# Optimization experiments

Hardware: AMD Instinct MI355X
Metric: run time of the kernel (lower is better)

## Reference

```python
import jax, jax.numpy as jnp
import numpy as np

M, DIM_X, DIM_Y, PROJ = 4096, 1024, 128, 128
BN_EPS = 1e-5


def setup_inputs() -> dict:
    key = jax.random.key(0)
    ks = jax.random.split(key, 4)
    x = jax.random.normal(ks[0], (M, DIM_X), dtype=jnp.float32)
    y = jax.random.normal(ks[1], (M, DIM_Y), dtype=jnp.float32)
    # BatchNorm1d affine params (init: gamma=1, beta=0)
    bnx_gamma = jnp.ones((DIM_X,), jnp.float32)
    bnx_beta = jnp.zeros((DIM_X,), jnp.float32)
    bny_gamma = jnp.ones((DIM_Y,), jnp.float32)
    bny_beta = jnp.zeros((DIM_Y,), jnp.float32)
    # Linear(dim_x, proj) params
    bound = 1.0 / np.sqrt(DIM_X)
    W = jax.random.uniform(ks[2], (PROJ, DIM_X), jnp.float32, -bound, bound)
    b = jax.random.uniform(ks[3], (PROJ,), jnp.float32, -bound, bound)
    return {"x": x, "y": y, "bnx_gamma": bnx_gamma, "bnx_beta": bnx_beta,
            "bny_gamma": bny_gamma, "bny_beta": bny_beta, "W": W, "b": b}


def _batchnorm(z, gamma, beta):
    # training-mode BatchNorm1d: biased variance over batch dim
    mu = z.mean(axis=0)
    var = z.var(axis=0)
    return (z - mu) * jax.lax.rsqrt(var + BN_EPS) * gamma + beta


def _pairwise_sq_dists(z):
    # -2 z z^T + |z_i|^2 + |z_j|^2  (same formula as the torch module)
    n2 = jnp.sum(z * z, axis=-1, keepdims=True)  # [m,1]
    return -2.0 * (z @ z.T) + n2 + n2.T          # [m,m]


def reference(x, y, bnx_gamma, bnx_beta, bny_gamma, bny_beta, W, b):
    m = x.shape[0]
    xn = _batchnorm(x, bnx_gamma, bnx_beta)
    yn = _batchnorm(y, bny_gamma, bny_beta)
    xp = xn @ W.T + b                              # projected x: [m, PROJ]

    pdx = _pairwise_sq_dists(xp)
    pdy = _pairwise_sq_dists(yn)
    # sigma = max(1e-6, median(pairwise distances).detach())
    sx = jnp.maximum(1e-6, jax.lax.stop_gradient(jnp.median(pdx)))
    sy = jnp.maximum(1e-6, jax.lax.stop_gradient(jnp.median(pdy)))

    K = jnp.exp(-pdx / sx)
    L = jnp.exp(-pdy / sy)
    # trace(L H K H) == sum(L * (H K H)) since L symmetric; H K H = double centering of K
    Kc = K - K.mean(axis=0, keepdims=True) - K.mean(axis=1, keepdims=True) + K.mean()
    hsic = jnp.sum(L * Kc) / ((m - 1) ** 2)
    return hsic
```

## Files before the change

### kernel.cpp

```cpp
#include <hip/hip_runtime.h>


constexpr int   MM  = 4096;
constexpr int   DX  = 1024;
constexpr int   DY  = 128;
constexpr int   PJ  = 128;
constexpr unsigned RANK0 = 8388607u;
constexpr unsigned RANK1 = 8388608u;
constexpr int   NTRI128 = 528;
constexpr int   NTRI64  = 2080;

typedef __attribute__((ext_vector_type(8))) short bf16x8;
typedef __attribute__((ext_vector_type(4))) float f32x4;

struct Ctrl {
  unsigned pref[2];
  unsigned rrank[2];
  float sigma;
  float coef;
};

__device__ __forceinline__ unsigned mapf(float f) {
  unsigned b = __float_as_uint(f);
  return (b & 0x80000000u) ? ~b : (b | 0x80000000u);
}
__device__ __forceinline__ float unmapf(unsigned u) {
  unsigned b = (u & 0x80000000u) ? (u & 0x7fffffffu) : ~u;
  return __uint_as_float(b);
}
__device__ __forceinline__ unsigned short f2bf(float f) {
  unsigned u = __float_as_uint(f);
  return (unsigned short)((u + 0x7fffu + ((u >> 16) & 1u)) >> 16);
}
__device__ __forceinline__ float bf2f(unsigned short h) {
  return __uint_as_float(((unsigned)h) << 16);
}
__device__ __forceinline__ void gload_lds16(const void* g, void* l) {
  __builtin_amdgcn_global_load_lds(
      (const __attribute__((address_space(1))) unsigned int*)g,
      (__attribute__((address_space(3))) unsigned int*)l, 16, 0, 0);
}
__device__ __forceinline__ void tri_map(int lin, int& bi, int& bj) {
  int b = (int)((sqrtf(8.0f * (float)lin + 1.0f) - 1.0f) * 0.5f);
  while ((b + 1) * (b + 2) / 2 <= lin) ++b;
  while (b * (b + 1) / 2 > lin) --b;
  bi = b;
  bj = lin - b * (b + 1) / 2;
}

__global__ void colstats(const float* __restrict__ x, const float* __restrict__ y,
                         double* __restrict__ sumx, double* __restrict__ sqx,
                         double* __restrict__ sumy, double* __restrict__ sqy) {
  const int r0 = blockIdx.y * 256;
  const float* src;
  double *sum, *sq;
  int col, ncols;
  if (blockIdx.x < 4) {
    col = blockIdx.x * 256 + threadIdx.x; ncols = DX; src = x; sum = sumx; sq = sqx;
  } else {
    col = threadIdx.x; ncols = DY; src = y; sum = sumy; sq = sqy;
    if (col >= DY) return;
  }
  const float* px = src + (size_t)r0 * ncols + col;
  double s = 0.0, s2 = 0.0;
  for (int r = 0; r < 256; ++r) {
    float v = *px;
    s  += (double)v;
    s2 += (double)v * (double)v;
    px += ncols;
  }
  atomicAdd(&sum[col], s);
  atomicAdd(&sq[col],  s2);
}

__global__ void finalize_stats(const double* __restrict__ sumx, const double* __restrict__ sqx,
                               const double* __restrict__ sumy, const double* __restrict__ sqy,
                               const float* __restrict__ gx, const float* __restrict__ bx,
                               const float* __restrict__ gy, const float* __restrict__ by,
                               float* __restrict__ axv, float* __restrict__ cxv,
                               float* __restrict__ ayv, float* __restrict__ cyv) {
  const double* sum; const double* sq; const float* gamma; const float* beta;
  float *a, *c; int j;
  if (blockIdx.x < 4) {
    j = blockIdx.x * 256 + threadIdx.x;
    sum = sumx; sq = sqx; gamma = gx; beta = bx; a = axv; c = cxv;
  } else {
    j = threadIdx.x;
    if (j >= DY) return;
    sum = sumy; sq = sqy; gamma = gy; beta = by; a = ayv; c = cyv;
  }
  double mu  = sum[j] * (1.0 / 4096.0);
  double var = sq[j] * (1.0 / 4096.0) - mu * mu;
  float rstd = (float)(1.0 / sqrt(var + 1e-5));
  float aj   = rstd * gamma[j];
  a[j] = aj;
  c[j] = beta[j] - (float)mu * aj;
}

__global__ __launch_bounds__(256) void prep(
    const float* __restrict__ x, const float* __restrict__ y,
    const float* __restrict__ W, const float* __restrict__ b,
    const float* __restrict__ ax, const float* __restrict__ cx,
    const float* __restrict__ ay, const float* __restrict__ cy,
    unsigned short* __restrict__ Ah, unsigned short* __restrict__ Al,
    unsigned short* __restrict__ Wh, unsigned short* __restrict__ Wl,
    unsigned short* __restrict__ Zhy, unsigned short* __restrict__ Zly,
    float* __restrict__ n2y, float* __restrict__ bp) {
  __shared__ float red[256];
  const int bx = blockIdx.x, tid = threadIdx.x;
  if (bx < 4096) {
    int i4 = bx * 256 + tid;
    float4 v = ((const float4*)x)[i4];
    int c0 = (i4 * 4) & 1023;
    v.x *= ax[c0]; v.y *= ax[c0 + 1]; v.z *= ax[c0 + 2]; v.w *= ax[c0 + 3];
    ushort4 h, lo;
    h.x = f2bf(v.x); h.y = f2bf(v.y); h.z = f2bf(v.z); h.w = f2bf(v.w);
    lo.x = f2bf(v.x - bf2f(h.x)); lo.y = f2bf(v.y - bf2f(h.y));
    lo.z = f2bf(v.z - bf2f(h.z)); lo.w = f2bf(v.w - bf2f(h.w));
    ((ushort4*)Ah)[i4] = h;
    ((ushort4*)Al)[i4] = lo;
  } else if (bx < 5120) {
    int wv = tid >> 6, lane = tid & 63;
    int row = (bx - 4096) * 4 + wv;
    size_t base = (size_t)row * 128;
    float v0 = y[base + lane]      * ay[lane]      + cy[lane];
    float v1 = y[base + 64 + lane] * ay[64 + lane] + cy[64 + lane];
    unsigned short h0 = f2bf(v0), h1 = f2bf(v1);
    Zhy[base + lane] = h0;            Zhy[base + 64 + lane] = h1;
    Zly[base + lane] = f2bf(v0 - bf2f(h0));
    Zly[base + 64 + lane] = f2bf(v1 - bf2f(h1));
    float s = v0 * v0 + v1 * v1;
    for (int off = 32; off > 0; off >>= 1) s += __shfl_down(s, off, 64);
    if (lane == 0) n2y[row] = s;
  } else if (bx < 5248) {
    int i4 = (bx - 5120) * 256 + tid;
    float4 v = ((const float4*)W)[i4];
    ushort4 h, lo;
    h.x = f2bf(v.x); h.y = f2bf(v.y); h.z = f2bf(v.z); h.w = f2bf(v.w);
    lo.x = f2bf(v.x - bf2f(h.x)); lo.y = f2bf(v.y - bf2f(h.y));
    lo.z = f2bf(v.z - bf2f(h.z)); lo.w = f2bf(v.w - bf2f(h.w));
    ((ushort4*)Wh)[i4] = h;
    ((ushort4*)Wl)[i4] = lo;
  } else {
    int p = bx - 5248;
    float s = 0.f;
    for (int j = tid; j < DX; j += 256) s += cx[j] * W[(size_t)p * DX + j];
    red[tid] = s; __syncthreads();
    for (int off = 128; off > 0; off >>= 1) {
      if (tid < off) red[tid] += red[tid + off];
      __syncthreads();
    }
    if (tid == 0) bp[p] = b[p] + red[0];
  }
}

template <int STRIDE>
__device__ __forceinline__ void stage_panel(const unsigned short* __restrict__ src,
                                            int r0, int k0, short* dst, int tid) {
  #pragma unroll
  for (int c = 0; c < 4; ++c) {
    int e     = c * 256 + tid;
    int row   = e >> 3;
    int inrow = (e & 7) << 4;
    int srcb  = inrow ^ ((row & 7) << 4);
    gload_lds16(src + (size_t)(r0 + row) * STRIDE + k0 + (srcb >> 1), &dst[e * 8]);
  }
}

__device__ __forceinline__ void mfma_tiles(const short* As, const short* Bs,
                                           int wr, int wc, int l, f32x4 (&acc)[4][4]) {
  #pragma unroll
  for (int ks = 0; ks < 2; ++ks) {
    bf16x8 af[4], bfr[4];
    #pragma unroll
    for (int mi = 0; mi < 4; ++mi) {
      int row   = wr * 64 + mi * 16 + (l & 15);
      int inrow = (ks * 64 + ((l >> 4) << 4)) ^ ((row & 7) << 4);
      af[mi] = *(const bf16x8*)&As[row * 64 + (inrow >> 1)];
    }
    #pragma unroll
    for (int ni = 0; ni < 4; ++ni) {
      int row   = wc * 64 + ni * 16 + (l & 15);
      int inrow = (ks * 64 + ((l >> 4) << 4)) ^ ((row & 7) << 4);
      bfr[ni] = *(const bf16x8*)&Bs[row * 64 + (inrow >> 1)];
    }
    #pragma unroll
    for (int mi = 0; mi < 4; ++mi)
      #pragma unroll
      for (int ni = 0; ni < 4; ++ni)
        acc[mi][ni] = __builtin_amdgcn_mfma_f32_16x16x32_bf16(af[mi], bfr[ni], acc[mi][ni], 0, 0, 0);
  }
}

__device__ __forceinline__ void stage64(const unsigned short* __restrict__ src,
                                        int r0, int k0, short* dst, int tid) {
  #pragma unroll
  for (int c = 0; c < 2; ++c) {
    int e     = c * 256 + tid;
    int row   = e >> 3;
    int inrow = (e & 7) << 4;
    int srcb  = inrow ^ ((row & 7) << 4);
    gload_lds16(src + (size_t)(r0 + row) * 128 + k0 + (srcb >> 1), &dst[e * 8]);
  }
}

__device__ __forceinline__ void mfma64(const short* As, const short* Bs,
                                       int wr, int wc, int l, f32x4 (&acc)[2][2]) {
  #pragma unroll
  for (int ks = 0; ks < 2; ++ks) {
    bf16x8 af[2], bfr[2];
    #pragma unroll
    for (int mi = 0; mi < 2; ++mi) {
      int row   = wr * 32 + mi * 16 + (l & 15);
      int inrow = (ks * 64 + ((l >> 4) << 4)) ^ ((row & 7) << 4);
      af[mi] = *(const bf16x8*)&As[row * 64 + (inrow >> 1)];
    }
    #pragma unroll
    for (int ni = 0; ni < 2; ++ni) {
      int row   = wc * 32 + ni * 16 + (l & 15);
      int inrow = (ks * 64 + ((l >> 4) << 4)) ^ ((row & 7) << 4);
      bfr[ni] = *(const bf16x8*)&Bs[row * 64 + (inrow >> 1)];
    }
    #pragma unroll
    for (int mi = 0; mi < 2; ++mi)
      #pragma unroll
      for (int ni = 0; ni < 2; ++ni)
        acc[mi][ni] = __builtin_amdgcn_mfma_f32_16x16x32_bf16(af[mi], bfr[ni], acc[mi][ni], 0, 0, 0);
  }
}

__global__ __launch_bounds__(256) void proj_part(
    const unsigned short* __restrict__ Ah, const unsigned short* __restrict__ Al,
    const unsigned short* __restrict__ Wh, const unsigned short* __restrict__ Wl,
    float* __restrict__ Pp) {
  __shared__ __align__(16) short smem[32768];
  const int tid = threadIdx.x;
  const int l   = tid & 63, w = tid >> 6;
  const int wr  = w >> 1, wc = w & 1;
  const int r0  = blockIdx.x * 128;
  const int s   = blockIdx.y;

  auto stage_ph = [&](int t, short* h) {
    int ktg  = s * 6 + t;
    int term = ktg >> 4, k0 = (ktg & 15) << 6;
    const unsigned short* sA = (term < 2) ? Ah : Al;
    const unsigned short* sB = (term == 1) ? Wl : Wh;
    stage_panel<1024>(sA, r0, k0, h, tid);
    stage_panel<1024>(sB, 0, k0, h + 8192, tid);
  };

  f32x4 acc[4][4] = {};
  stage_ph(0, smem);
  asm volatile("s_waitcnt vmcnt(0)" ::: "memory");
  __syncthreads();
  for (int t = 0; t < 6; ++t) {
    short* h = smem + (t & 1) * 16384;
    if (t < 5) stage_ph(t + 1, smem + ((t + 1) & 1) * 16384);
    mfma_tiles(h, h + 8192, wr, wc, l, acc);
    asm volatile("s_waitcnt vmcnt(0)" ::: "memory");
    __syncthreads();
  }
  float* out = Pp + (size_t)s * (MM * PJ);
  #pragma unroll
  for (int mi = 0; mi < 4; ++mi)
    #pragma unroll
    for (int ni = 0; ni < 4; ++ni)
      #pragma unroll
      for (int r = 0; r < 4; ++r) {
        int i = r0 + wr * 64 + mi * 16 + ((l >> 4) << 2) + r;
        int j = wc * 64 + ni * 16 + (l & 15);
        out[(size_t)i * PJ + j] = acc[mi][ni][r];
      }
}

__global__ void proj_finish(const float* __restrict__ Pp, const float* __restrict__ bp,
                            unsigned short* __restrict__ Zh, unsigned short* __restrict__ Zl,
                            float* __restrict__ n2x) {
  int wv = threadIdx.x >> 6, lane = threadIdx.x & 63;
  int row = blockIdx.x * 4 + wv;
  size_t base = (size_t)row * 128;
  float v0 = bp[lane], v1 = bp[64 + lane];
  #pragma unroll
  for (int s = 0; s < 8; ++s) {
    v0 += Pp[(size_t)s * (MM * PJ) + base + lane];
    v1 += Pp[(size_t)s * (MM * PJ) + base + 64 + lane];
  }
  unsigned short h0 = f2bf(v0), h1 = f2bf(v1);
  Zh[base + lane] = h0;            Zh[base + 64 + lane] = h1;
  Zl[base + lane] = f2bf(v0 - bf2f(h0));
  Zl[base + 64 + lane] = f2bf(v1 - bf2f(h1));
  float s2 = v0 * v0 + v1 * v1;
  for (int off = 32; off > 0; off >>= 1) s2 += __shfl_down(s2, off, 64);
  if (lane == 0) n2x[row] = s2;
}

__global__ __launch_bounds__(256) void gram_hist_pd(
    const unsigned short* __restrict__ Zhx, const unsigned short* __restrict__ Zlx,
    const unsigned short* __restrict__ Zhy, const unsigned short* __restrict__ Zly,
    const float* __restrict__ n2x, const float* __restrict__ n2y,
    unsigned* __restrict__ ghx, unsigned* __restrict__ ghy,
    unsigned* __restrict__ pd) {
  __shared__ __align__(16) short smem[32768];
  int bi, bj;
  tri_map(blockIdx.x, bi, bj);
  const int z = blockIdx.y;
  const unsigned short* Zh = z ? Zhy : Zhx;
  const unsigned short* Zl = z ? Zly : Zlx;
  const float* n2 = z ? n2y : n2x;
  unsigned* gh = z ? ghy : ghx;
  const int r0 = bi * 128, c0 = bj * 128;

  const int tid = threadIdx.x;
  const int l   = tid & 63, w = tid >> 6;
  const int wr  = w >> 1, wc = w & 1;

  auto stage_ph = [&](int kt, short* h) {
    const unsigned short* srcA = (kt < 4) ? Zh : Zl;
    const unsigned short* srcB = (kt < 2 || kt >= 4) ? Zh : Zl;
    const int k0 = (kt & 1) * 64;
    stage_panel<128>(srcA, r0, k0, h, tid);
    stage_panel<128>(srcB, c0, k0, h + 8192, tid);
  };

  f32x4 acc[4][4] = {};
  stage_ph(0, smem);
  asm volatile("s_waitcnt vmcnt(0)" ::: "memory");
  __syncthreads();
  for (int kt = 0; kt < 6; ++kt) {
    short* h = smem + (kt & 1) * 16384;
    if (kt < 5) stage_ph(kt + 1, smem + ((kt + 1) & 1) * 16384);
    mfma_tiles(h, h + 8192, wr, wc, l, acc);
    asm volatile("s_waitcnt vmcnt(0)" ::: "memory");
    __syncthreads();
  }

  unsigned* lh = (unsigned*)smem;
  for (int t = tid; t < 8192; t += 256) lh[t] = 0u;
  __syncthreads();

  const unsigned inc = (bi == bj) ? 1u : 2u;
  unsigned* pdt = pd + ((size_t)z * NTRI128 + blockIdx.x) * 16384;

  float n2i[4][4], n2j[4];
  #pragma unroll
  for (int mi = 0; mi < 4; ++mi)
    #pragma unroll
    for (int r = 0; r < 4; ++r)
      n2i[mi][r] = n2[r0 + wr * 64 + mi * 16 + ((l >> 4) << 2) + r];
  #pragma unroll
  for (int ni = 0; ni < 4; ++ni) n2j[ni] = n2[c0 + wc * 64 + ni * 16 + (l & 15)];

  #pragma unroll
  for (int mi = 0; mi < 4; ++mi) {
    #pragma unroll
    for (int ni = 0; ni < 4; ++ni) {
      uint4 uv;
      #pragma unroll
      for (int r = 0; r < 4; ++r) {
        float pdv = n2i[mi][r] + n2j[ni] - 2.0f * acc[mi][ni][r];
        unsigned u = mapf(pdv);
        ((unsigned*)&uv)[r] = u;
        unsigned bin = u >> 20;
        atomicAdd(&lh[((bin & 2047u) << 2) | (unsigned)(l & 3)],
                  inc << ((bin >> 11) << 4));
      }
      *(uint4*)&pdt[(mi * 4 + ni) * 1024 + tid * 4] = uv;
    }
  }
  __syncthreads();
  for (int t = tid; t < 4096; t += 256) {
    unsigned idx = (unsigned)(t & 2047) << 2;
    int sh = (t >> 11) << 4;
    unsigned v = ((lh[idx]     >> sh) & 0xffffu)
               + ((lh[idx | 1] >> sh) & 0xffffu)
               + ((lh[idx | 2] >> sh) & 0xffffu)
               + ((lh[idx | 3] >> sh) & 0xffffu);
    if (v) atomicAdd(&gh[t], v);
  }
}

__global__ __launch_bounds__(256) void pd_hist2(
    const unsigned* __restrict__ pd,
    const Ctrl* __restrict__ ctrlx, const Ctrl* __restrict__ ctrly,
    unsigned* __restrict__ part) {
  __shared__ unsigned lh[8192];
  const int tid = threadIdx.x, z = blockIdx.y;
  int bi, bj;
  tri_map(blockIdx.x, bi, bj);
  const Ctrl* ctrl = z ? ctrly : ctrlx;
  const unsigned p0 = ctrl->pref[0], p1 = ctrl->pref[1];
  const unsigned inc = (bi == bj) ? 1u : 2u;
  const uint4* pt = (const uint4*)(pd + ((size_t)z * NTRI128 + blockIdx.x) * 16384);
  for (int t = tid; t < 8192; t += 256) lh[t] = 0u;
  __syncthreads();
  #pragma unroll 4
  for (int it = 0; it < 16; ++it) {
    uint4 uv = pt[it * 256 + tid];
    #pragma unroll
    for (int e = 0; e < 4; ++e) {
      unsigned u = ((const unsigned*)&uv)[e];
      unsigned top = u >> 20, mid = (u >> 8) & 4095u;
      if (top == p0) atomicAdd(&lh[mid], inc);
      if (top == p1) atomicAdd(&lh[4096 + mid], inc);
    }
  }
  __syncthreads();
  unsigned* dst = part + ((size_t)z * NTRI128 + blockIdx.x) * 4096;
  for (int t = tid; t < 4096; t += 256)
    dst[t] = (lh[2 * t] & 0xffffu) | (lh[2 * t + 1] << 16);
}

__global__ __launch_bounds__(256) void pd_kl(
    const unsigned* __restrict__ pdx, const unsigned* __restrict__ pdy,
    const Ctrl* __restrict__ ctrlx, const Ctrl* __restrict__ ctrly,
    double* __restrict__ colK, double* __restrict__ colL, double* __restrict__ S1) {
  __shared__ float rowKs[128], rowLs[128], colKs[128], colLs[128];
  __shared__ float red[256];
  int bi, bj;
  tri_map(blockIdx.x, bi, bj);
  const int r0 = bi * 128, c0 = bj * 128;
  const bool diag = (bi == bj);
  const int tid = threadIdx.x;
  const int l = tid & 63, w = tid >> 6;
  const int wr = w >> 1, wc = w & 1;
  const int vh = blockIdx.y;
  const float fx = ctrlx->coef, fy = ctrly->coef;
  const uint4* ptx = (const uint4*)(pdx + (size_t)blockIdx.x * 16384);
  const uint4* pty = (const uint4*)(pdy + (size_t)blockIdx.x * 16384);
  if (tid < 128) { rowKs[tid] = 0.f; rowLs[tid] = 0.f; colKs[tid] = 0.f; colLs[tid] = 0.f; }
  __syncthreads();
  float s1 = 0.f;
  float cK[4] = {}, cL[4] = {};
  #pragma unroll
  for (int m = 0; m < 2; ++m) {
    int mi = vh * 2 + m;
    float rkK[4] = {}, rkL[4] = {};
    #pragma unroll
    for (int ni = 0; ni < 4; ++ni) {
      uint4 ux = ptx[(mi * 4 + ni) * 256 + tid];
      uint4 uy = pty[(mi * 4 + ni) * 256 + tid];
      #pragma unroll
      for (int r = 0; r < 4; ++r) {
        float Kv = exp2f(unmapf(((const unsigned*)&ux)[r]) * fx);
        float Lv = exp2f(unmapf(((const unsigned*)&uy)[r]) * fy);
        s1 += Kv * Lv;
        rkK[r] += Kv; rkL[r] += Lv;
        cK[ni] += Kv; cL[ni] += Lv;
      }
    }
    #pragma unroll
    for (int r = 0; r < 4; ++r) {
      int il = wr * 64 + mi * 16 + ((l >> 4) << 2) + r;
      float rk = rkK[r], rl = rkL[r];
      rk += __shfl_xor(rk, 1); rk += __shfl_xor(rk, 2);
      rk += __shfl_xor(rk, 4); rk += __shfl_xor(rk, 8);
      rl += __shfl_xor(rl, 1); rl += __shfl_xor(rl, 2);
      rl += __shfl_xor(rl, 4); rl += __shfl_xor(rl, 8);
      if ((l & 15) == 0) {
        atomicAdd(&rowKs[il], rk);
        atomicAdd(&rowLs[il], rl);
      }
    }
  }
  #pragma unroll
  for (int ni = 0; ni < 4; ++ni) {
    float ck = cK[ni], cl = cL[ni];
    ck += __shfl_xor(ck, 16); ck += __shfl_xor(ck, 32);
    cl += __shfl_xor(cl, 16); cl += __shfl_xor(cl, 32);
    if (l < 16) {
      int jl = wc * 64 + ni * 16 + l;
      atomicAdd(&colKs[jl], ck);
      atomicAdd(&colLs[jl], cl);
    }
  }
  red[tid] = s1;
  __syncthreads();
  for (int off = 128; off > 0; off >>= 1) {
    if (tid < off) red[tid] += red[tid + off];
    __syncthreads();
  }
  if (tid == 0) atomicAdd(S1, (double)red[0] * (diag ? 1.0 : 2.0));
  if (tid < 128) {
    atomicAdd(&colK[c0 + tid], (double)colKs[tid]);
    atomicAdd(&colL[c0 + tid], (double)colLs[tid]);
    if (!diag) {
      atomicAdd(&colK[r0 + tid], (double)rowKs[tid]);
      atomicAdd(&colL[r0 + tid], (double)rowLs[tid]);
    }
  }
}

template <int MODE>
__global__ __launch_bounds__(256) void gram_hist(
    const unsigned short* __restrict__ Zhx, const unsigned short* __restrict__ Zlx,
    const unsigned short* __restrict__ Zhy, const unsigned short* __restrict__ Zly,
    const float* __restrict__ n2x, const float* __restrict__ n2y,
    const Ctrl* __restrict__ ctrlx, const Ctrl* __restrict__ ctrly,
    unsigned* __restrict__ ghx, unsigned* __restrict__ ghy,
    unsigned* __restrict__ part) {
  __shared__ __align__(16) short smem[32768];
  int bi, bj;
  tri_map(blockIdx.x, bi, bj);
  const int z = blockIdx.y;
  const unsigned short* Zh = z ? Zhy : Zhx;
  const unsigned short* Zl = z ? Zly : Zlx;
  const float* n2 = z ? n2y : n2x;
  const Ctrl* ctrl = z ? ctrly : ctrlx;
  unsigned* gh = z ? ghy : ghx;
  const int r0 = bi * 128, c0 = bj * 128;

  const int tid = threadIdx.x;
  const int l   = tid & 63, w = tid >> 6;
  const int wr  = w >> 1, wc = w & 1;

  auto stage_ph = [&](int kt, short* h) {
    const unsigned short* srcA = (kt < 4) ? Zh : Zl;
    const unsigned short* srcB = (kt < 2 || kt >= 4) ? Zh : Zl;
    const int k0 = (kt & 1) * 64;
    stage_panel<128>(srcA, r0, k0, h, tid);
    stage_panel<128>(srcB, c0, k0, h + 8192, tid);
  };

  f32x4 acc[4][4] = {};
  stage_ph(0, smem);
  asm volatile("s_waitcnt vmcnt(0)" ::: "memory");
  __syncthreads();
  for (int kt = 0; kt < 6; ++kt) {
    short* h = smem + (kt & 1) * 16384;
    if (kt < 5) stage_ph(kt + 1, smem + ((kt + 1) & 1) * 16384);
    mfma_tiles(h, h + 8192, wr, wc, l, acc);
    asm volatile("s_waitcnt vmcnt(0)" ::: "memory");
    __syncthreads();
  }

  unsigned* lh = (unsigned*)smem;
  for (int t = tid; t < 8192; t += 256) lh[t] = 0u;
  __syncthreads();

  unsigned p0 = 0, p1 = 0;
  if constexpr (MODE == 2) { p0 = ctrl->pref[0]; p1 = ctrl->pref[1]; }
  const unsigned inc = (bi == bj) ? 1u : 2u;

  float n2i[4][4], n2j[4];
  #pragma unroll
  for (int mi = 0; mi < 4; ++mi)
    #pragma unroll
    for (int r = 0; r < 4; ++r)
      n2i[mi][r] = n2[r0 + wr * 64 + mi * 16 + ((l >> 4) << 2) + r];
  #pragma unroll
  for (int ni = 0; ni < 4; ++ni) n2j[ni] = n2[c0 + wc * 64 + ni * 16 + (l & 15)];

  #pragma unroll
  for (int mi = 0; mi < 4; ++mi) {
    #pragma unroll
    for (int ni = 0; ni < 4; ++ni) {
      #pragma unroll
      for (int r = 0; r < 4; ++r) {
        float pdv = n2i[mi][r] + n2j[ni] - 2.0f * acc[mi][ni][r];
        unsigned u = mapf(pdv);
        if constexpr (MODE == 1) {
          unsigned bin = u >> 20;
          atomicAdd(&lh[((bin & 2047u) << 2) | (unsigned)(l & 3)],
                    inc << ((bin >> 11) << 4));
        } else {
          unsigned top = u >> 20, mid = (u >> 8) & 4095u;
          if (top == p0) atomicAdd(&lh[mid], inc);
          if (top == p1) atomicAdd(&lh[4096 + mid], inc);
        }
      }
    }
  }
  __syncthreads();
  if constexpr (MODE == 1) {
    for (int t = tid; t < 4096; t += 256) {
      unsigned idx = (unsigned)(t & 2047) << 2;
      int sh = (t >> 11) << 4;
      unsigned v = ((lh[idx]     >> sh) & 0xffffu)
                 + ((lh[idx | 1] >> sh) & 0xffffu)
                 + ((lh[idx | 2] >> sh) & 0xffffu)
                 + ((lh[idx | 3] >> sh) & 0xffffu);
      if (v) atomicAdd(&gh[t], v);
    }
  } else {
    unsigned* dst = part + ((size_t)z * NTRI128 + blockIdx.x) * 4096;
    for (int t = tid; t < 4096; t += 256)
      dst[t] = (lh[2 * t] & 0xffffu) | (lh[2 * t + 1] << 16);
  }
}

__global__ void hist2_reduce(const unsigned* __restrict__ part,
                             unsigned* __restrict__ ghx, unsigned* __restrict__ ghy) {
  const int t = blockIdx.x * 256 + threadIdx.x;
  const int z = blockIdx.y;
  const int b0 = blockIdx.z * 66;
  const int nb = (b0 + 66 <= NTRI128) ? 66 : (NTRI128 - b0);
  const unsigned* p = part + ((size_t)z * NTRI128 + b0) * 4096;
  unsigned s0 = 0, s1 = 0;
  for (int b = 0; b < nb; ++b) {
    unsigned v = p[(size_t)b * 4096 + t];
    s0 += v & 0xffffu;
    s1 += v >> 16;
  }
  unsigned* gh = z ? ghy : ghx;
  if (s0) atomicAdd(&gh[2 * t], s0);
  if (s1) atomicAdd(&gh[2 * t + 1], s1);
}

__global__ __launch_bounds__(256) void gram_kl(
    const unsigned short* __restrict__ Zhx, const unsigned short* __restrict__ Zlx,
    const unsigned short* __restrict__ Zhy, const unsigned short* __restrict__ Zly,
    const float* __restrict__ n2x, const float* __restrict__ n2y,
    const Ctrl* __restrict__ ctrlx, const Ctrl* __restrict__ ctrly,
    double* __restrict__ colK, double* __restrict__ colL, double* __restrict__ S1) {
  __shared__ __align__(16) short smem[8192];
  int bi, bj;
  tri_map(blockIdx.x, bi, bj);
  const int r0 = bi * 64, c0 = bj * 64;
  const bool diag = (bi == bj);
  const int tid = threadIdx.x;
  const int l   = tid & 63, w = tid >> 6;
  const int wr  = w >> 1, wc = w & 1;
  short* As = smem;
  short* Bs = smem + 4096;

  f32x4 accx[2][2] = {};
  f32x4 accy[2][2] = {};
  #pragma unroll
  for (int m = 0; m < 2; ++m) {
    const unsigned short* Zh = m ? Zhy : Zhx;
    const unsigned short* Zl = m ? Zly : Zlx;
    for (int kt = 0; kt < 6; ++kt) {
      const unsigned short* sA = (kt < 4) ? Zh : Zl;
      const unsigned short* sB = (kt < 2 || kt >= 4) ? Zh : Zl;
      const int k0 = (kt & 1) * 64;
      stage64(sA, r0, k0, As, tid);
      stage64(sB, c0, k0, Bs, tid);
      asm volatile("s_waitcnt vmcnt(0)" ::: "memory");
      __syncthreads();
      if (m == 0) mfma64(As, Bs, wr, wc, l, accx);
      else        mfma64(As, Bs, wr, wc, l, accy);
      __syncthreads();
    }
  }

  float* rowKs = (float*)smem;
  float* rowLs = rowKs + 64;
  float* colKs = rowLs + 64;
  float* colLs = colKs + 64;
  float* red   = colLs + 64;
  ((float*)smem)[tid] = 0.f;
  __syncthreads();

  const float fx = ctrlx->coef, fy = ctrly->coef;
  float s1 = 0.f;
  float cK[2] = {0.f, 0.f}, cL[2] = {0.f, 0.f};
  #pragma unroll
  for (int mi = 0; mi < 2; ++mi) {
    #pragma unroll
    for (int r = 0; r < 4; ++r) {
      int il = wr * 32 + mi * 16 + ((l >> 4) << 2) + r;
      int i  = r0 + il;
      float rk = 0.f, rl = 0.f;
      #pragma unroll
      for (int ni = 0; ni < 2; ++ni) {
        int j = c0 + wc * 32 + ni * 16 + (l & 15);
        float Kv = exp2f((n2x[i] + n2x[j] - 2.0f * accx[mi][ni][r]) * fx);
        float Lv = exp2f((n2y[i] + n2y[j] - 2.0f * accy[mi][ni][r]) * fy);
        s1 += Kv * Lv;
        rk += Kv; rl += Lv;
        cK[ni] += Kv; cL[ni] += Lv;
      }
      rk += __shfl_xor(rk, 1); rk += __shfl_xor(rk, 2);
      rk += __shfl_xor(rk, 4); rk += __shfl_xor(rk, 8);
      rl += __shfl_xor(rl, 1); rl += __shfl_xor(rl, 2);
      rl += __shfl_xor(rl, 4); rl += __shfl_xor(rl, 8);
      if ((l & 15) == 0) {
        atomicAdd(&rowKs[il], rk);
        atomicAdd(&rowLs[il], rl);
      }
    }
  }
  #pragma unroll
  for (int ni = 0; ni < 2; ++ni) {
    float ck = cK[ni], cl = cL[ni];
    ck += __shfl_xor(ck, 16); ck += __shfl_xor(ck, 32);
    cl += __shfl_xor(cl, 16); cl += __shfl_xor(cl, 32);
    if (l < 16) {
      int jl = wc * 32 + ni * 16 + l;
      atomicAdd(&colKs[jl], ck);
      atomicAdd(&colLs[jl], cl);
    }
  }
  red[tid] = s1;
  __syncthreads();
  for (int off = 128; off > 0; off >>= 1) {
    if (tid < off) red[tid] += red[tid + off];
    __syncthreads();
  }
  if (tid == 0) atomicAdd(S1, (double)red[0] * (diag ? 1.0 : 2.0));
  if (tid < 64) {
    atomicAdd(&colK[c0 + tid], (double)colKs[tid]);
    atomicAdd(&colL[c0 + tid], (double)colLs[tid]);
    if (!diag) {
      atomicAdd(&colK[r0 + tid], (double)rowKs[tid]);
      atomicAdd(&colL[r0 + tid], (double)rowLs[tid]);
    }
  }
}

template <int SEG>
__global__ void scan_select(const unsigned* __restrict__ hxa, const unsigned* __restrict__ hya,
                            int qstride, Ctrl* ctrlx, Ctrl* ctrly, int level) {
  __shared__ unsigned part[256];
  __shared__ unsigned s_bin[2];
  const int tid = threadIdx.x;
  for (int m = 0; m < 2; ++m) {
    const unsigned* hbase = m ? hya : hxa;
    Ctrl* ctrl = m ? ctrly : ctrlx;
    for (int q = 0; q < 2; ++q) {
      const unsigned* h = hbase + q * qstride;
      unsigned rank = (level == 1) ? ((q == 0) ? RANK0 : RANK1) : ctrl->rrank[q];
      unsigned loc[SEG];
      unsigned s = 0;
      #pragma unroll
      for (int b = 0; b < SEG; ++b) { loc[b] = h[tid * SEG + b]; s += loc[b]; }
      part[tid] = s; __syncthreads();
      for (int off = 1; off < 256; off <<= 1) {
        unsigned t = (tid >= off) ? part[tid - off] : 0u;
        __syncthreads();
        part[tid] += t;
        __syncthreads();
      }
      unsigned pre = part[tid] - s;
      if (rank >= pre && rank < pre + s) {
        unsigned cum = pre;
        #pragma unroll
        for (int b = 0; b < SEG; ++b) {
          if (rank < cum + loc[b]) {
            s_bin[q] = tid * SEG + b;
            if (level == 1) ctrl->rrank[q] = rank - cum;
            break;
          }
          cum += loc[b];
        }
      }
      __syncthreads();
    }
    if (level == 1) {
      if (tid < 2) ctrl->pref[tid] = s_bin[tid];
    } else {
      if (tid == 0) {
        unsigned u0 = (((ctrl->pref[0] << 12) | s_bin[0]) << 8) + 128u;
        unsigned u1 = (((ctrl->pref[1] << 12) | s_bin[1]) << 8) + 128u;
        float med = 0.5f * (unmapf(u0) + unmapf(u1));
        float sig = fmaxf(1e-6f, med);
        ctrl->sigma = sig;
        ctrl->coef  = -1.4426950408889634f / sig;
      }
    }
    __syncthreads();
  }
}

__global__ void finalize_hsic(const double* __restrict__ colK, const double* __restrict__ colL,
                              const double* __restrict__ S1, float* __restrict__ out) {
  __shared__ double rk[256], rl[256], rkl[256];
  double tk = 0.0, tl = 0.0, tkl = 0.0;
  for (int i = threadIdx.x; i < MM; i += 256) {
    double k = colK[i], l = colL[i];
    tk += k; tl += l; tkl += k * l;
  }
  rk[threadIdx.x] = tk; rl[threadIdx.x] = tl; rkl[threadIdx.x] = tkl;
  __syncthreads();
  for (int off = 128; off > 0; off >>= 1) {
    if (threadIdx.x < off) {
      rk[threadIdx.x]  += rk[threadIdx.x + off];
      rl[threadIdx.x]  += rl[threadIdx.x + off];
      rkl[threadIdx.x] += rkl[threadIdx.x + off];
    }
    __syncthreads();
  }
  if (threadIdx.x == 0) {
    double m = 4096.0;
    double s = S1[0] - (2.0 / m) * rkl[0] + rk[0] * rl[0] / (m * m);
    out[0] = (float)(s / (4095.0 * 4095.0));
  }
}

extern "C" void kernel_launch(void* const* d_in, const int* in_sizes, int n_in,
                              void* d_out, int out_size, void* d_ws, size_t ws_size,
                              hipStream_t stream) {
  const float* x   = (const float*)d_in[0];
  const float* y   = (const float*)d_in[1];
  const float* bxg = (const float*)d_in[2];
  const float* bxb = (const float*)d_in[3];
  const float* byg = (const float*)d_in[4];
  const float* byb = (const float*)d_in[5];
  const float* W   = (const float*)d_in[6];
  const float* b   = (const float*)d_in[7];
  float* out = (float*)d_out;

  char* w = (char*)d_ws;
  unsigned short* Ah  = (unsigned short*)(w);
  unsigned short* Al  = (unsigned short*)(w + 8388608ull);
  unsigned short* Wh  = (unsigned short*)(w + 16777216ull);
  unsigned short* Wl  = (unsigned short*)(w + 17039360ull);
  unsigned short* Zhx = (unsigned short*)(w + 17301504ull);
  unsigned short* Zlx = (unsigned short*)(w + 18350080ull);
  unsigned short* Zhy = (unsigned short*)(w + 19398656ull);
  unsigned short* Zly = (unsigned short*)(w + 20447232ull);
  float*          Pp  = (float*)(w + 21495808ull);
  unsigned*       part = (unsigned*)(w);
  size_t ZR = 21495808ull + 16777216ull;
  double*   sumx = (double*)(w + ZR);
  double*   sqx  = sumx + 1024;
  double*   sumy = sqx + 1024;
  double*   sqy  = sumy + 128;
  unsigned* h1x  = (unsigned*)(sqy + 128);
  unsigned* h1y  = h1x + 4096;
  unsigned* h2x  = h1y + 4096;
  unsigned* h2y  = h2x + 8192;
  double*   colK = (double*)(h2y + 8192);
  double*   colL = colK + 4096;
  double*   S1   = colL + 4096;
  size_t zero_bytes = (size_t)((char*)(S1 + 1) - (w + ZR));
  size_t PR = ZR + ((zero_bytes + 255ull) & ~255ull);
  float* ax  = (float*)(w + PR);
  float* cx  = ax + 1024;
  float* ay  = cx + 1024;
  float* cy  = ay + 128;
  float* bp  = cy + 128;
  float* n2x = bp + 128;
  float* n2y = n2x + 4096;
  Ctrl* ctrlx = (Ctrl*)(n2y + 4096);
  Ctrl* ctrly = ctrlx + 1;

  constexpr size_t PD0     = 41943040ull;
  constexpr size_t PD_ELEM = (size_t)NTRI128 * 16384;
  constexpr size_t WS_FAST = PD0 + 2ull * PD_ELEM * 4ull;
  unsigned* pdx = (unsigned*)(w + PD0);
  unsigned* pdy = pdx + PD_ELEM;
  const bool fast = (ws_size >= WS_FAST);

  hipMemsetAsync(w + ZR, 0, zero_bytes, stream);

  colstats<<<dim3(5, 16), 256, 0, stream>>>(x, y, sumx, sqx, sumy, sqy);
  finalize_stats<<<5, 256, 0, stream>>>(sumx, sqx, sumy, sqy, bxg, bxb, byg, byb,
                                        ax, cx, ay, cy);
  prep<<<5376, 256, 0, stream>>>(x, y, W, b, ax, cx, ay, cy,
                                 Ah, Al, Wh, Wl, Zhy, Zly, n2y, bp);
  proj_part<<<dim3(32, 8), 256, 0, stream>>>(Ah, Al, Wh, Wl, Pp);
  proj_finish<<<1024, 256, 0, stream>>>(Pp, bp, Zhx, Zlx, n2x);

  if (fast) {
    gram_hist_pd<<<dim3(NTRI128, 2), 256, 0, stream>>>(Zhx, Zlx, Zhy, Zly, n2x, n2y,
                                                       h1x, h1y, pdx);
    scan_select<16><<<1, 256, 0, stream>>>(h1x, h1y, 0, ctrlx, ctrly, 1);
    pd_hist2<<<dim3(NTRI128, 2), 256, 0, stream>>>(pdx, ctrlx, ctrly, part);
    hist2_reduce<<<dim3(16, 2, 8), 256, 0, stream>>>(part, h2x, h2y);
    scan_select<16><<<1, 256, 0, stream>>>(h2x, h2y, 4096, ctrlx, ctrly, 2);
    pd_kl<<<dim3(NTRI128, 2), 256, 0, stream>>>(pdx, pdy, ctrlx, ctrly,
                                                colK, colL, S1);
  } else {
    gram_hist<1><<<dim3(NTRI128, 2), 256, 0, stream>>>(Zhx, Zlx, Zhy, Zly, n2x, n2y,
                                                       ctrlx, ctrly, h1x, h1y, part);
    scan_select<16><<<1, 256, 0, stream>>>(h1x, h1y, 0, ctrlx, ctrly, 1);
    gram_hist<2><<<dim3(NTRI128, 2), 256, 0, stream>>>(Zhx, Zlx, Zhy, Zly, n2x, n2y,
                                                       ctrlx, ctrly, h2x, h2y, part);
    hist2_reduce<<<dim3(16, 2, 8), 256, 0, stream>>>(part, h2x, h2y);
    scan_select<16><<<1, 256, 0, stream>>>(h2x, h2y, 4096, ctrlx, ctrly, 2);
    gram_kl<<<NTRI64, 256, 0, stream>>>(Zhx, Zlx, Zhy, Zly, n2x, n2y,
                                        ctrlx, ctrly, colK, colL, S1);
  }
  finalize_hsic<<<1, 256, 0, stream>>>(colK, colL, S1, out);
}
```

Measured before the change: 164.6 us.

## Reorder split-bf16 GEMM stages across four LDS panels and merge duplicate histogram bins

The pairwise-distance GEMM used to restage both A and B panels for each of six hi/lo k-steps in a double buffer. It now keeps four 128x64 panels in shared memory and reuses loaded hi/lo panels across several MFMA passes, so fewer global loads and barriers are needed. Separately, each thread now merges equal histogram bins among its four values before issuing LDS atomics, which cuts contended atomics when neighbouring distances fall in the same bin. The manual schedule is fragile, and the dedup logic adds compare instructions to the epilogue.

After: 171.1 us. 3.9% more time.

```diff
diff --git a/kernel.cpp b/kernel.cpp
--- a/kernel.cpp
+++ b/kernel.cpp
@@ -314,25 +314,37 @@
   const int l   = tid & 63, w = tid >> 6;
   const int wr  = w >> 1, wc = w & 1;
 
-  auto stage_ph = [&](int kt, short* h) {
-    const unsigned short* srcA = (kt < 4) ? Zh : Zl;
-    const unsigned short* srcB = (kt < 2 || kt >= 4) ? Zh : Zl;
-    const int k0 = (kt & 1) * 64;
-    stage_panel<128>(srcA, r0, k0, h, tid);
-    stage_panel<128>(srcB, c0, k0, h + 8192, tid);
-  };
+  short* S0 = smem;
+  short* S1 = smem + 8192;
+  short* S2 = smem + 16384;
+  short* S3 = smem + 24576;
 
   f32x4 acc[4][4] = {};
-  stage_ph(0, smem);
+  stage_panel<128>(Zh, r0, 0, S0, tid);
+  stage_panel<128>(Zh, c0, 0, S1, tid);
+  stage_panel<128>(Zl, c0, 0, S2, tid);
   asm volatile("s_waitcnt vmcnt(0)" ::: "memory");
   __syncthreads();
-  for (int kt = 0; kt < 6; ++kt) {
-    short* h = smem + (kt & 1) * 16384;
-    if (kt < 5) stage_ph(kt + 1, smem + ((kt + 1) & 1) * 16384);
-    mfma_tiles(h, h + 8192, wr, wc, l, acc);
-    asm volatile("s_waitcnt vmcnt(0)" ::: "memory");
-    __syncthreads();
-  }
+  stage_panel<128>(Zl, r0, 0, S3, tid);
+  mfma_tiles(S0, S1, wr, wc, l, acc);
+  asm volatile("s_waitcnt vmcnt(0)" ::: "memory");
+  __syncthreads();
+  mfma_tiles(S0, S2, wr, wc, l, acc);
+  __syncthreads();
+  stage_panel<128>(Zh, r0, 64, S0, tid);
+  stage_panel<128>(Zh, c0, 64, S2, tid);
+  mfma_tiles(S3, S1, wr, wc, l, acc);
+  asm volatile("s_waitcnt vmcnt(0)" ::: "memory");
+  __syncthreads();
+  stage_panel<128>(Zl, c0, 64, S1, tid);
+  stage_panel<128>(Zl, r0, 64, S3, tid);
+  mfma_tiles(S0, S2, wr, wc, l, acc);
+  asm volatile("s_waitcnt vmcnt(0)" ::: "memory");
+  __syncthreads();
+  mfma_tiles(S0, S1, wr, wc, l, acc);
+  __syncthreads();
+  mfma_tiles(S3, S2, wr, wc, l, acc);
+  __syncthreads();
 
   unsigned* lh = (unsigned*)smem;
   for (int t = tid; t < 8192; t += 256) lh[t] = 0u;
@@ -355,16 +367,28 @@
     #pragma unroll
     for (int ni = 0; ni < 4; ++ni) {
       uint4 uv;
+      unsigned bb[4];
+      unsigned cnt[4] = {inc, inc, inc, inc};
       #pragma unroll
       for (int r = 0; r < 4; ++r) {
         float pdv = n2i[mi][r] + n2j[ni] - 2.0f * acc[mi][ni][r];
         unsigned u = mapf(pdv);
         ((unsigned*)&uv)[r] = u;
-        unsigned bin = u >> 20;
-        atomicAdd(&lh[((bin & 2047u) << 2) | (unsigned)(l & 3)],
-                  inc << ((bin >> 11) << 4));
+        bb[r] = u >> 20;
       }
       *(uint4*)&pdt[(mi * 4 + ni) * 1024 + tid * 4] = uv;
+      #pragma unroll
+      for (int r = 3; r >= 1; --r) {
+        #pragma unroll
+        for (int s = 0; s < r; ++s) {
+          if (bb[r] == bb[s]) { cnt[s] += cnt[r]; cnt[r] = 0; break; }
+        }
+      }
+      #pragma unroll
+      for (int r = 0; r < 4; ++r)
+        if (cnt[r])
+          atomicAdd(&lh[((bb[r] & 2047u) << 2) | (unsigned)(l & 3)],
+                    cnt[r] << ((bb[r] >> 11) << 4));
     }
   }
   __syncthreads();
```

## Use 512-thread blocks for gram/pd kernels and split scan_select per matrix

Applied to the files above, without the earlier changes.

The Gram-plus-histogram kernel and the exp/KL kernel now run 8 waves per 128x128 tile instead of 4. Each wave owns a 64x32 sub-tile, and the pd tile store layout is changed to match. pd_kl drops its two-way blockIdx.y split and covers all four row groups in one block. scan_select now runs one block per matrix (x and y in parallel), and level 1 does a single histogram scan that finds both median ranks. Together this adds parallelism and removes serial scan work, at the cost of higher register and LDS pressure per block and fewer blocks for pd_kl.

Result: faster. 152.2 us (-7.6%).

```diff
diff --git a/kernel.cpp b/kernel.cpp
--- a/kernel.cpp
+++ b/kernel.cpp
@@ -167,6 +167,19 @@
   }
 }
 
+template <int STRIDE>
+__device__ __forceinline__ void stage_panel2(const unsigned short* __restrict__ src,
+                                             int r0, int k0, short* dst, int tid) {
+  #pragma unroll
+  for (int c = 0; c < 2; ++c) {
+    int e     = c * 512 + tid;
+    int row   = e >> 3;
+    int inrow = (e & 7) << 4;
+    int srcb  = inrow ^ ((row & 7) << 4);
+    gload_lds16(src + (size_t)(r0 + row) * STRIDE + k0 + (srcb >> 1), &dst[e * 8]);
+  }
+}
+
 __device__ __forceinline__ void mfma_tiles(const short* As, const short* Bs,
                                            int wr, int wc, int l, f32x4 (&acc)[4][4]) {
   #pragma unroll
@@ -188,6 +201,31 @@
     for (int mi = 0; mi < 4; ++mi)
       #pragma unroll
       for (int ni = 0; ni < 4; ++ni)
+        acc[mi][ni] = __builtin_amdgcn_mfma_f32_16x16x32_bf16(af[mi], bfr[ni], acc[mi][ni], 0, 0, 0);
+  }
+}
+
+__device__ __forceinline__ void mfma_tiles8(const short* As, const short* Bs,
+                                            int wr, int wc, int l, f32x4 (&acc)[4][2]) {
+  #pragma unroll
+  for (int ks = 0; ks < 2; ++ks) {
+    bf16x8 af[4], bfr[2];
+    #pragma unroll
+    for (int mi = 0; mi < 4; ++mi) {
+      int row   = wr * 64 + mi * 16 + (l & 15);
+      int inrow = (ks * 64 + ((l >> 4) << 4)) ^ ((row & 7) << 4);
+      af[mi] = *(const bf16x8*)&As[row * 64 + (inrow >> 1)];
+    }
+    #pragma unroll
+    for (int ni = 0; ni < 2; ++ni) {
+      int row   = wc * 32 + ni * 16 + (l & 15);
+      int inrow = (ks * 64 + ((l >> 4) << 4)) ^ ((row & 7) << 4);
+      bfr[ni] = *(const bf16x8*)&Bs[row * 64 + (inrow >> 1)];
+    }
+    #pragma unroll
+    for (int mi = 0; mi < 4; ++mi)
+      #pragma unroll
+      for (int ni = 0; ni < 2; ++ni)
         acc[mi][ni] = __builtin_amdgcn_mfma_f32_16x16x32_bf16(af[mi], bfr[ni], acc[mi][ni], 0, 0, 0);
   }
 }
@@ -294,7 +332,7 @@
   if (lane == 0) n2x[row] = s2;
 }
 
-__global__ __launch_bounds__(256) void gram_hist_pd(
+__global__ __launch_bounds__(512) void gram_hist_pd(
     const unsigned short* __restrict__ Zhx, const unsigned short* __restrict__ Zlx,
     const unsigned short* __restrict__ Zhy, const unsigned short* __restrict__ Zly,
     const float* __restrict__ n2x, const float* __restrict__ n2y,
@@ -312,48 +350,48 @@
 
   const int tid = threadIdx.x;
   const int l   = tid & 63, w = tid >> 6;
-  const int wr  = w >> 1, wc = w & 1;
+  const int wr  = w >> 2, wc = w & 3;
 
   auto stage_ph = [&](int kt, short* h) {
     const unsigned short* srcA = (kt < 4) ? Zh : Zl;
     const unsigned short* srcB = (kt < 2 || kt >= 4) ? Zh : Zl;
     const int k0 = (kt & 1) * 64;
-    stage_panel<128>(srcA, r0, k0, h, tid);
-    stage_panel<128>(srcB, c0, k0, h + 8192, tid);
+    stage_panel2<128>(srcA, r0, k0, h, tid);
+    stage_panel2<128>(srcB, c0, k0, h + 8192, tid);
   };
 
-  f32x4 acc[4][4] = {};
+  f32x4 acc[4][2] = {};
   stage_ph(0, smem);
   asm volatile("s_waitcnt vmcnt(0)" ::: "memory");
   __syncthreads();
   for (int kt = 0; kt < 6; ++kt) {
     short* h = smem + (kt & 1) * 16384;
     if (kt < 5) stage_ph(kt + 1, smem + ((kt + 1) & 1) * 16384);
-    mfma_tiles(h, h + 8192, wr, wc, l, acc);
+    mfma_tiles8(h, h + 8192, wr, wc, l, acc);
     asm volatile("s_waitcnt vmcnt(0)" ::: "memory");
     __syncthreads();
   }
 
   unsigned* lh = (unsigned*)smem;
-  for (int t = tid; t < 8192; t += 256) lh[t] = 0u;
+  for (int t = tid; t < 8192; t += 512) lh[t] = 0u;
   __syncthreads();
 
   const unsigned inc = (bi == bj) ? 1u : 2u;
   unsigned* pdt = pd + ((size_t)z * NTRI128 + blockIdx.x) * 16384;
 
-  float n2i[4][4], n2j[4];
+  float n2i[4][4], n2j[2];
   #pragma unroll
   for (int mi = 0; mi < 4; ++mi)
     #pragma unroll
     for (int r = 0; r < 4; ++r)
       n2i[mi][r] = n2[r0 + wr * 64 + mi * 16 + ((l >> 4) << 2) + r];
   #pragma unroll
-  for (int ni = 0; ni < 4; ++ni) n2j[ni] = n2[c0 + wc * 64 + ni * 16 + (l & 15)];
+  for (int ni = 0; ni < 2; ++ni) n2j[ni] = n2[c0 + wc * 32 + ni * 16 + (l & 15)];
 
   #pragma unroll
   for (int mi = 0; mi < 4; ++mi) {
     #pragma unroll
-    for (int ni = 0; ni < 4; ++ni) {
+    for (int ni = 0; ni < 2; ++ni) {
       uint4 uv;
       #pragma unroll
       for (int r = 0; r < 4; ++r) {
@@ -364,11 +402,11 @@
         atomicAdd(&lh[((bin & 2047u) << 2) | (unsigned)(l & 3)],
                   inc << ((bin >> 11) << 4));
       }
-      *(uint4*)&pdt[(mi * 4 + ni) * 1024 + tid * 4] = uv;
-    }
-  }
-  __syncthreads();
-  for (int t = tid; t < 4096; t += 256) {
+      *(uint4*)&pdt[(mi * 2 + ni) * 2048 + tid * 4] = uv;
+    }
+  }
+  __syncthreads();
+  for (int t = tid; t < 4096; t += 512) {
     unsigned idx = (unsigned)(t & 2047) << 2;
     int sh = (t >> 11) << 4;
     unsigned v = ((lh[idx]     >> sh) & 0xffffu)
@@ -410,35 +448,33 @@
     dst[t] = (lh[2 * t] & 0xffffu) | (lh[2 * t + 1] << 16);
 }
 
-__global__ __launch_bounds__(256) void pd_kl(
+__global__ __launch_bounds__(512) void pd_kl(
     const unsigned* __restrict__ pdx, const unsigned* __restrict__ pdy,
     const Ctrl* __restrict__ ctrlx, const Ctrl* __restrict__ ctrly,
     double* __restrict__ colK, double* __restrict__ colL, double* __restrict__ S1) {
   __shared__ float rowKs[128], rowLs[128], colKs[128], colLs[128];
-  __shared__ float red[256];
+  __shared__ float red[512];
   int bi, bj;
   tri_map(blockIdx.x, bi, bj);
   const int r0 = bi * 128, c0 = bj * 128;
   const bool diag = (bi == bj);
   const int tid = threadIdx.x;
   const int l = tid & 63, w = tid >> 6;
-  const int wr = w >> 1, wc = w & 1;
-  const int vh = blockIdx.y;
+  const int wr = w >> 2, wc = w & 3;
   const float fx = ctrlx->coef, fy = ctrly->coef;
   const uint4* ptx = (const uint4*)(pdx + (size_t)blockIdx.x * 16384);
   const uint4* pty = (const uint4*)(pdy + (size_t)blockIdx.x * 16384);
   if (tid < 128) { rowKs[tid] = 0.f; rowLs[tid] = 0.f; colKs[tid] = 0.f; colLs[tid] = 0.f; }
   __syncthreads();
   float s1 = 0.f;
-  float cK[4] = {}, cL[4] = {};
-  #pragma unroll
-  for (int m = 0; m < 2; ++m) {
-    int mi = vh * 2 + m;
+  float cK[2] = {}, cL[2] = {};
+  #pragma unroll
+  for (int mi = 0; mi < 4; ++mi) {
     float rkK[4] = {}, rkL[4] = {};
     #pragma unroll
-    for (int ni = 0; ni < 4; ++ni) {
-      uint4 ux = ptx[(mi * 4 + ni) * 256 + tid];
-      uint4 uy = pty[(mi * 4 + ni) * 256 + tid];
+    for (int ni = 0; ni < 2; ++ni) {
+      uint4 ux = ptx[(mi * 2 + ni) * 512 + tid];
+      uint4 uy = pty[(mi * 2 + ni) * 512 + tid];
       #pragma unroll
       for (int r = 0; r < 4; ++r) {
         float Kv = exp2f(unmapf(((const unsigned*)&ux)[r]) * fx);
@@ -463,19 +499,19 @@
     }
   }
   #pragma unroll
-  for (int ni = 0; ni < 4; ++ni) {
+  for (int ni = 0; ni < 2; ++ni) {
     float ck = cK[ni], cl = cL[ni];
     ck += __shfl_xor(ck, 16); ck += __shfl_xor(ck, 32);
     cl += __shfl_xor(cl, 16); cl += __shfl_xor(cl, 32);
     if (l < 16) {
-      int jl = wc * 64 + ni * 16 + l;
+      int jl = wc * 32 + ni * 16 + l;
       atomicAdd(&colKs[jl], ck);
       atomicAdd(&colLs[jl], cl);
     }
   }
   red[tid] = s1;
   __syncthreads();
-  for (int off = 128; off > 0; off >>= 1) {
+  for (int off = 256; off > 0; off >>= 1) {
     if (tid < off) red[tid] += red[tid + off];
     __syncthreads();
   }
@@ -714,51 +750,66 @@
   __shared__ unsigned part[256];
   __shared__ unsigned s_bin[2];
   const int tid = threadIdx.x;
-  for (int m = 0; m < 2; ++m) {
-    const unsigned* hbase = m ? hya : hxa;
-    Ctrl* ctrl = m ? ctrly : ctrlx;
-    for (int q = 0; q < 2; ++q) {
-      const unsigned* h = hbase + q * qstride;
-      unsigned rank = (level == 1) ? ((q == 0) ? RANK0 : RANK1) : ctrl->rrank[q];
-      unsigned loc[SEG];
-      unsigned s = 0;
+  const int m = blockIdx.x;
+  const unsigned* hbase = m ? hya : hxa;
+  Ctrl* ctrl = m ? ctrly : ctrlx;
+  const int nq = (level == 1) ? 1 : 2;
+  for (int q = 0; q < nq; ++q) {
+    const unsigned* h = hbase + q * qstride;
+    unsigned loc[SEG];
+    unsigned s = 0;
+    #pragma unroll
+    for (int b = 0; b < SEG; ++b) { loc[b] = h[tid * SEG + b]; s += loc[b]; }
+    part[tid] = s; __syncthreads();
+    for (int off = 1; off < 256; off <<= 1) {
+      unsigned t = (tid >= off) ? part[tid - off] : 0u;
+      __syncthreads();
+      part[tid] += t;
+      __syncthreads();
+    }
+    unsigned pre = part[tid] - s;
+    if (level == 1) {
       #pragma unroll
-      for (int b = 0; b < SEG; ++b) { loc[b] = h[tid * SEG + b]; s += loc[b]; }
-      part[tid] = s; __syncthreads();
-      for (int off = 1; off < 256; off <<= 1) {
-        unsigned t = (tid >= off) ? part[tid - off] : 0u;
-        __syncthreads();
-        part[tid] += t;
-        __syncthreads();
+      for (int qq = 0; qq < 2; ++qq) {
+        unsigned rank = qq ? RANK1 : RANK0;
+        if (rank >= pre && rank < pre + s) {
+          unsigned cum = pre;
+          #pragma unroll
+          for (int b = 0; b < SEG; ++b) {
+            if (rank < cum + loc[b]) {
+              s_bin[qq] = tid * SEG + b;
+              ctrl->rrank[qq] = rank - cum;
+              break;
+            }
+            cum += loc[b];
+          }
+        }
       }
-      unsigned pre = part[tid] - s;
+    } else {
+      unsigned rank = ctrl->rrank[q];
       if (rank >= pre && rank < pre + s) {
         unsigned cum = pre;
         #pragma unroll
         for (int b = 0; b < SEG; ++b) {
           if (rank < cum + loc[b]) {
             s_bin[q] = tid * SEG + b;
-            if (level == 1) ctrl->rrank[q] = rank - cum;
             break;
           }
           cum += loc[b];
         }
       }
-      __syncthreads();
-    }
-    if (level == 1) {
-      if (tid < 2) ctrl->pref[tid] = s_bin[tid];
-    } else {
-      if (tid == 0) {
-        unsigned u0 = (((ctrl->pref[0] << 12) | s_bin[0]) << 8) + 128u;
-        unsigned u1 = (((ctrl->pref[1] << 12) | s_bin[1]) << 8) + 128u;
-        float med = 0.5f * (unmapf(u0) + unmapf(u1));
-        float sig = fmaxf(1e-6f, med);
-        ctrl->sigma = sig;
-        ctrl->coef  = -1.4426950408889634f / sig;
-      }
     }
     __syncthreads();
+  }
+  if (level == 1) {
+    if (tid < 2) ctrl->pref[tid] = s_bin[tid];
+  } else if (tid == 0) {
+    unsigned u0 = (((ctrl->pref[0] << 12) | s_bin[0]) << 8) + 128u;
+    unsigned u1 = (((ctrl->pref[1] << 12) | s_bin[1]) << 8) + 128u;
+    float med = 0.5f * (unmapf(u0) + unmapf(u1));
+    float sig = fmaxf(1e-6f, med);
+    ctrl->sigma = sig;
+    ctrl->coef  = -1.4426950408889634f / sig;
   }
 }
 
@@ -853,22 +904,22 @@
   proj_finish<<<1024, 256, 0, stream>>>(Pp, bp, Zhx, Zlx, n2x);
 
   if (fast) {
-    gram_hist_pd<<<dim3(NTRI128, 2), 256, 0, stream>>>(Zhx, Zlx, Zhy, Zly, n2x, n2y,
+    gram_hist_pd<<<dim3(NTRI128, 2), 512, 0, stream>>>(Zhx, Zlx, Zhy, Zly, n2x, n2y,
                                                        h1x, h1y, pdx);
-    scan_select<16><<<1, 256, 0, stream>>>(h1x, h1y, 0, ctrlx, ctrly, 1);
+    scan_select<16><<<2, 256, 0, stream>>>(h1x, h1y, 0, ctrlx, ctrly, 1);
     pd_hist2<<<dim3(NTRI128, 2), 256, 0, stream>>>(pdx, ctrlx, ctrly, part);
     hist2_reduce<<<dim3(16, 2, 8), 256, 0, stream>>>(part, h2x, h2y);
-    scan_select<16><<<1, 256, 0, stream>>>(h2x, h2y, 4096, ctrlx, ctrly, 2);
-    pd_kl<<<dim3(NTRI128, 2), 256, 0, stream>>>(pdx, pdy, ctrlx, ctrly,
-                                                colK, colL, S1);
+    scan_select<16><<<2, 256, 0, stream>>>(h2x, h2y, 4096, ctrlx, ctrly, 2);
+    pd_kl<<<NTRI128, 512, 0, stream>>>(pdx, pdy, ctrlx, ctrly,
+                                       colK, colL, S1);
   } else {
     gram_hist<1><<<dim3(NTRI128, 2), 256, 0, stream>>>(Zhx, Zlx, Zhy, Zly, n2x, n2y,
                                                        ctrlx, ctrly, h1x, h1y, part);
-    scan_select<16><<<1, 256, 0, stream>>>(h1x, h1y, 0, ctrlx, ctrly, 1);
+    scan_select<16><<<2, 256, 0, stream>>>(h1x, h1y, 0, ctrlx, ctrly, 1);
     gram_hist<2><<<dim3(NTRI128, 2), 256, 0, stream>>>(Zhx, Zlx, Zhy, Zly, n2x, n2y,
                                                        ctrlx, ctrly, h2x, h2y, part);
     hist2_reduce<<<dim3(16, 2, 8), 256, 0, stream>>>(part, h2x, h2y);
-    scan_select<16><<<1, 256, 0, stream>>>(h2x, h2y, 4096, ctrlx, ctrly, 2);
+    scan_select<16><<<2, 256, 0, stream>>>(h2x, h2y, 4096, ctrlx, ctrly, 2);
     gram_kl<<<NTRI64, 256, 0, stream>>>(Zhx, Zlx, Zhy, Zly, n2x, n2y,
                                         ctrlx, ctrly, colK, colL, S1);
   }
```
